# Optimization experiments

Hardware: AMD Instinct MI355X
Metric: run time of the kernel (lower is better)

The kernel has to match this reference:

```python
import jax, jax.numpy as jnp
import numpy as np

B, N, P, D = 16, 1024, 72, 96
ND, H, K = 64, 4, 16
LN_EPS = 1e-5
ROW_EPS = 1e-8


def topk_sparsify(adj, k):
    # adj: (..., N, N); keep top-k per row (scatter-mask), then row-renormalize
    shp = adj.shape
    n = shp[-1]
    flat = adj.reshape(-1, n)
    _, idx = jax.lax.top_k(flat, k)  # (R, k)
    rows = jnp.arange(flat.shape[0])[:, None]
    mask = jnp.zeros_like(flat).at[rows, idx].set(1.0)
    sp = flat * mask
    sp = sp / (sp.sum(-1, keepdims=True) + ROW_EPS)
    return sp.reshape(shp)


def setup_inputs() -> dict:
    key = jax.random.key(0)
    ks = jax.random.split(key, 12)
    xav1 = np.sqrt(6.0 / (N + ND))  # xavier_uniform bound for (N, ND)
    inp = {
        "patch_features": jax.random.normal(ks[0], (B, N, P, D), jnp.float32),
        "E1": jax.random.uniform(ks[1], (H, N, ND), jnp.float32, -xav1, xav1),
        "E2": jax.random.uniform(ks[2], (H, ND, N), jnp.float32, -xav1, xav1),
        "temperature": jnp.full((H,), 0.5, jnp.float32),
        "fusion_weight": jnp.float32(0.5),
        "dW1": jax.random.normal(ks[3], (D, ND), jnp.float32) / np.sqrt(D),
        "db1": jnp.zeros((ND,), jnp.float32),
        "ln_g": jnp.ones((ND,), jnp.float32),
        "ln_b": jnp.zeros((ND,), jnp.float32),
        "dW2": jax.random.normal(ks[4], (ND, ND), jnp.float32) / np.sqrt(ND),
        "db2": jnp.zeros((ND,), jnp.float32),
        "eW1": jax.random.normal(ks[5], (H, 2 * H), jnp.float32) / np.sqrt(H),
        "eb1": jnp.zeros((2 * H,), jnp.float32),
        "eW2": jax.random.normal(ks[6], (2 * H, 1), jnp.float32) / np.sqrt(2 * H),
        "eb2": jnp.zeros((1,), jnp.float32),
    }
    return inp


def reference(patch_features, E1, E2, temperature, fusion_weight,
              dW1, db1, ln_g, ln_b, dW2, db2, eW1, eb1, eW2, eb2):
    # ---- static multi-head graphs: softmax(relu(E1 @ E2) / T, axis=-1) ----
    s = jax.nn.relu(jnp.einsum('hnd,hdm->hnm', E1, E2))
    static_adjs = jax.nn.softmax(s / temperature[:, None, None], axis=-1)

    # ---- dynamic graphs from mean-pooled patch features ----
    node_repr = patch_features.mean(axis=2)                 # (B, N, D)
    h1 = node_repr @ dW1 + db1                              # (B, N, ND)
    mu = h1.mean(-1, keepdims=True)
    var = ((h1 - mu) ** 2).mean(-1, keepdims=True)
    h1 = (h1 - mu) / jnp.sqrt(var + LN_EPS) * ln_g + ln_b   # LayerNorm
    h1 = jax.nn.relu(h1)                                    # (dropout = identity, eval)
    dyn_emb = h1 @ dW2 + db2                                # (B, N, ND)
    d = jax.nn.relu(jnp.einsum('bnd,hdm->bhnm', dyn_emb, E2))
    dynamic_adjs = jax.nn.softmax(d / temperature[None, :, None, None], axis=-1)

    # ---- top-k sparsify + row renormalize ----
    static_adjs = topk_sparsify(static_adjs, K)             # (H, N, N)
    dynamic_adjs = topk_sparsify(dynamic_adjs, K)           # (B, H, N, N)

    # ---- fuse static + dynamic ----
    fused = (1.0 - fusion_weight) * static_adjs[None] + fusion_weight * dynamic_adjs

    # ---- edge MLP over head dim: (B, N, N, H) -> (B, N, N) ----
    x = jnp.transpose(fused, (0, 2, 3, 1))                  # (B, N, N, H)
    ew = jax.nn.relu(x @ eW1 + eb1) @ eW2 + eb2             # (B, N, N, 1)
    final_adjs = jax.nn.sigmoid(ew[..., 0]) * fused.mean(axis=1)
    return final_adjs, static_adjs, dynamic_adjs
```

## Files before the change

kernel.cpp:

```cpp
#include <hip/hip_runtime.h>

typedef unsigned int u32;
typedef unsigned long long u64;

#define Bn 16
#define Nn 1024
#define Pp 72
#define MARG 3e-4f

#define NEGINF __int_as_float(0xff800000)
#define POSINF __int_as_float(0x7f800000)

#define DPP_STEP(OP, CTRL, RM)                                                 \
  y = __builtin_amdgcn_update_dpp(__float_as_int(v), __float_as_int(v),        \
                                  CTRL, RM, 0xf, false);                       \
  v = OP(v, __int_as_float(y));

#define DPP_RED(NAME, OP)                                                      \
  __device__ __forceinline__ float NAME(float v) {                             \
    int y;                                                                     \
    DPP_STEP(OP, 0x111, 0xf)                                                   \
    DPP_STEP(OP, 0x112, 0xf)                                                   \
    DPP_STEP(OP, 0x114, 0xf)                                                   \
    DPP_STEP(OP, 0x118, 0xf)                                                   \
    DPP_STEP(OP, 0x142, 0xa)                                                   \
    DPP_STEP(OP, 0x143, 0xc)                                                   \
    return __int_as_float(__builtin_amdgcn_readlane(__float_as_int(v), 63));   \
  }

#define FADDOP(a, b) ((a) + (b))
DPP_RED(dmaxf, fmaxf)
DPP_RED(dminf, fminf)
DPP_RED(dsumf, FADDOP)

__device__ __forceinline__ u32 wminu(u32 v) {
#pragma unroll
  for (int off = 1; off < 64; off <<= 1) {
    u32 o = (u32)__shfl_xor((int)v, off, 64);
    v = (o < v) ? o : v;
  }
  return v;
}

template <int MODE>
__device__ __forceinline__ void select_row(const float* __restrict__ q,
                                           float* __restrict__ v, int l,
                                           const float* __restrict__ e1row,
                                           const double* __restrict__ edrow,
                                           const float* __restrict__ e2t,
                                           double Td) {
  float lm = q[0];
#pragma unroll
  for (int j = 1; j < 16; ++j) lm = fmaxf(lm, q[j]);
  const float qmax = dmaxf(lm);

  u32 lo = 0u, hi = __float_as_uint(qmax) + 1u;
  u32 kept = 0u;
  bool f16 = false;
  float pvf = 0.0f;
#pragma unroll 1
  while (hi - lo > 1u) {
    u32 mid = (lo + hi) >> 1;
    float pv = __uint_as_float(mid);
    u32 cw = 0;
#pragma unroll
    for (int j = 0; j < 16; ++j)
      cw += (u32)__popcll(__ballot(q[j] >= pv));
    if (cw >= 16u) lo = mid; else hi = mid;
    if (cw == 16u) { f16 = true; pvf = pv; break; }
  }
  float theta, ub;
  if (f16) {
    float vmin = POSINF, umax = -1.0f;
#pragma unroll
    for (int j = 0; j < 16; ++j) {
      if (q[j] >= pvf) { kept |= 1u << j; vmin = fminf(vmin, q[j]); }
      else umax = fmaxf(umax, q[j]);
    }
    theta = dminf(vmin);
    ub = dmaxf(umax);
  } else {
    theta = __uint_as_float(lo);
    u32 cw = 0;
#pragma unroll
    for (int j = 0; j < 16; ++j) {
      cw += (u32)__popcll(__ballot(q[j] > theta));
      if (q[j] > theta) kept |= 1u << j;
    }
    int rr = 16 - (int)cw;
#pragma unroll 1
    for (int it = 0; it < rr; ++it) {
      u32 mc = 0xFFFFFFFFu;
#pragma unroll
      for (int j = 0; j < 16; ++j)
        if (q[j] == theta && !((kept >> j) & 1u)) {
          u32 cc = (u32)((j << 6) | l);
          mc = cc < mc ? cc : mc;
        }
      u32 wm = wminu(mc);
      if ((wm & 63u) == (u32)l) kept |= 1u << (wm >> 6);
    }
    ub = theta;
  }

  if (theta - ub >= MARG) {
    float e[16];
    float es = 0.0f, ek = 0.0f;
#pragma unroll
    for (int j = 0; j < 16; ++j) {
      e[j] = __expf(q[j] - qmax);
      es += e[j];
      if ((kept >> j) & 1u) ek += e[j];
    }
    const float Z = dsumf(es);
    const float EK = dsumf(ek);
    const float inv = 1.0f / (EK + 1e-8f * Z);
#pragma unroll
    for (int j = 0; j < 16; ++j)
      v[j] = ((kept >> j) & 1u) ? (e[j] * inv) : 0.0f;
  } else {
    double qd[16];
    const float thr = ub - MARG;
#pragma unroll 1
    for (int j = 0; j < 16; ++j) {
      if (q[j] >= thr) {
        const int m = l + (j << 6);
        const float* col = e2t + (size_t)m * 64;
        double a = 0.0;
        for (int d = 0; d < 64; ++d) {
          double s = (MODE == 0) ? (double)e1row[d] : edrow[d];
          a = fma(s, (double)col[d], a);
        }
        qd[j] = (a > 0.0 ? a : 0.0) / Td;
      } else {
        qd[j] = (double)q[j];
      }
    }
    double bm = qd[0];
#pragma unroll
    for (int j = 1; j < 16; ++j) bm = qd[j] > bm ? qd[j] : bm;
    float mh = (float)bm;
    float mlo = (float)(bm - (double)mh);
    float whi = dmaxf(mh);
    float wlo = dmaxf(mh == whi ? mlo : NEGINF);
    const double qmaxd = (double)whi + (double)wlo;

    float ev2[16];
    float es2 = 0.0f;
#pragma unroll
    for (int j = 0; j < 16; ++j) { ev2[j] = __expf((float)(qd[j] - qmaxd)); es2 += ev2[j]; }
    const float Z2 = dsumf(es2);

    u32 kept2 = 0;
    float EK2 = 0.0f;
#pragma unroll 1
    for (int it = 0; it < 16; ++it) {
      double bv = -1.0;
      int bjj = -1;
#pragma unroll
      for (int j = 0; j < 16; ++j) {
        bool tk = (((kept2 >> j) & 1u) == 0u) && (qd[j] > bv);
        bv = tk ? qd[j] : bv;
        bjj = tk ? j : bjj;
      }
      float bh = NEGINF, bl = NEGINF;
      if (bjj >= 0) { bh = (float)bv; bl = (float)(bv - (double)bh); }
      float vhi = dmaxf(bh);
      float vlo = dmaxf(bh == vhi ? bl : NEGINF);
      bool elig = (bh == vhi) && (bl == vlo);
      u32 mc = elig ? (u32)((bjj << 6) | l) : 0xFFFFFFFFu;
      u32 mwin = wminu(mc);
      EK2 += __expf((float)(((double)vhi + (double)vlo) - qmaxd));
      if ((mwin & 63u) == (u32)l) kept2 |= 1u << (mwin >> 6);
    }
    const float inv2 = 1.0f / (EK2 + 1e-8f * Z2);
#pragma unroll
    for (int j = 0; j < 16; ++j)
      v[j] = ((kept2 >> j) & 1u) ? (ev2[j] * inv2) : 0.0f;
  }
}

__global__ __launch_bounds__(256) void k_e2t(const float* __restrict__ E2,
                                             float* __restrict__ E2T) {
  __shared__ float tile[32][65];
  const int h = blockIdx.x >> 5;
  const int m0 = (blockIdx.x & 31) << 5;
  const float* src = E2 + (size_t)h * 65536;
  float* dst = E2T + (size_t)h * 65536;
  const int t = threadIdx.x;
#pragma unroll
  for (int k = 0; k < 8; ++k) {
    int idx = k * 256 + t;
    int d = idx >> 5, mm = idx & 31;
    tile[mm][d] = src[d * 1024 + m0 + mm];
  }
  __syncthreads();
#pragma unroll
  for (int k = 0; k < 8; ++k) {
    int idx = k * 256 + t;
    int mm = idx >> 6, d = idx & 63;
    dst[(size_t)(m0 + mm) * 64 + d] = tile[mm][d];
  }
}

__global__ __launch_bounds__(128) void k_meanmlp(const float* __restrict__ pf,
                                                 const float* __restrict__ dW1,
                                                 const float* __restrict__ db1,
                                                 const float* __restrict__ ln_g,
                                                 const float* __restrict__ ln_b,
                                                 const float* __restrict__ dW2,
                                                 const float* __restrict__ db2,
                                                 double* __restrict__ embD,
                                                 float* __restrict__ embF) {
  __shared__ double ndD[96];
  __shared__ double red[64];
  __shared__ double h1r[64];
  const int t = threadIdx.x;
  const int bn = blockIdx.x;

  if (t < 96) {
    const float* src = pf + (size_t)bn * (Pp * 96) + t;
    double s = 0.0;
    for (int p = 0; p < Pp; ++p) s += (double)src[p * 96];
    ndD[t] = s / 72.0;
  }
  __syncthreads();

  double a = 0.0;
  if (t < 64) {
    a = (double)db1[t];
    for (int d = 0; d < 96; ++d) a = fma(ndD[d], (double)dW1[d * 64 + t], a);
    red[t] = a;
  }
  __syncthreads();
  for (int s2 = 32; s2 >= 1; s2 >>= 1) {
    if (t < s2) red[t] += red[t + s2];
    __syncthreads();
  }
  const double mu = red[0] * (1.0 / 64.0);
  __syncthreads();
  const double dv = a - mu;
  if (t < 64) red[t] = dv * dv;
  __syncthreads();
  for (int s2 = 32; s2 >= 1; s2 >>= 1) {
    if (t < s2) red[t] += red[t + s2];
    __syncthreads();
  }
  const double var = red[0] * (1.0 / 64.0);
  if (t < 64) {
    double xn = dv / sqrt(var + 1e-5) * (double)ln_g[t] + (double)ln_b[t];
    h1r[t] = xn > 0.0 ? xn : 0.0;
  }
  __syncthreads();
  if (t < 64) {
    double e = (double)db2[t];
    for (int k = 0; k < 64; ++k) e = fma(h1r[k], (double)dW2[k * 64 + t], e);
    embD[(size_t)bn * 64 + t] = e;
    embF[(size_t)bn * 64 + t] = (float)e;
  }
}

template <int MODE>
__global__ __launch_bounds__(256) void k_dot(const float* __restrict__ e1f,
                                             const float* __restrict__ embF,
                                             const float* __restrict__ E2,
                                             const float* __restrict__ temp,
                                             float* __restrict__ outp) {
  __shared__ float embsh[64][16];
  const int t = threadIdx.x;
  const int r0 = blockIdx.x * 16;
  int h;
  size_t erow;
  if (MODE == 0) {
    h = r0 >> 10;
    erow = (size_t)r0;
  } else {
    int b = r0 >> 12;
    h = (r0 >> 10) & 3;
    int n0 = r0 & 1023;
    erow = (size_t)(b << 10) + n0;
  }
  const float* efa = (MODE == 0) ? (e1f + erow * 64) : (embF + erow * 64);
  const float* e2 = E2 + (size_t)h * 65536;
  const float invT = 1.0f / temp[h];

#pragma unroll
  for (int i = t; i < 1024; i += 256) {
    int g = i & 15, d = i >> 4;
    embsh[d][g] = efa[g * 64 + d];
  }
  __syncthreads();

  const int s = t >> 7;
  const int c1 = (t & 127) * 4;
  const int c2 = c1 + 512;

  float acc[8][8];
#pragma unroll
  for (int g = 0; g < 8; ++g)
#pragma unroll
    for (int x = 0; x < 8; ++x) acc[g][x] = 0.0f;

#pragma unroll 4
  for (int d = 0; d < 64; ++d) {
    float4 va = *(const float4*)(e2 + d * 1024 + c1);
    float4 vb = *(const float4*)(e2 + d * 1024 + c2);
    float4 ea = *(const float4*)&embsh[d][8 * s];
    float4 eb = *(const float4*)&embsh[d][8 * s + 4];
    float sg;
#define ROWFMA(g, SS)                                                          \
    sg = SS;                                                                   \
    acc[g][0] = fmaf(sg, va.x, acc[g][0]);                                     \
    acc[g][1] = fmaf(sg, va.y, acc[g][1]);                                     \
    acc[g][2] = fmaf(sg, va.z, acc[g][2]);                                     \
    acc[g][3] = fmaf(sg, va.w, acc[g][3]);                                     \
    acc[g][4] = fmaf(sg, vb.x, acc[g][4]);                                     \
    acc[g][5] = fmaf(sg, vb.y, acc[g][5]);                                     \
    acc[g][6] = fmaf(sg, vb.z, acc[g][6]);                                     \
    acc[g][7] = fmaf(sg, vb.w, acc[g][7]);
    ROWFMA(0, ea.x) ROWFMA(1, ea.y) ROWFMA(2, ea.z) ROWFMA(3, ea.w)
    ROWFMA(4, eb.x) ROWFMA(5, eb.y) ROWFMA(6, eb.z) ROWFMA(7, eb.w)
#undef ROWFMA
  }

#pragma unroll
  for (int g = 0; g < 8; ++g) {
    float* orow = outp + (size_t)(r0 + 8 * s + g) * 1024;
    float4 o1, o2;
    o1.x = fmaxf(acc[g][0], 0.0f) * invT;
    o1.y = fmaxf(acc[g][1], 0.0f) * invT;
    o1.z = fmaxf(acc[g][2], 0.0f) * invT;
    o1.w = fmaxf(acc[g][3], 0.0f) * invT;
    o2.x = fmaxf(acc[g][4], 0.0f) * invT;
    o2.y = fmaxf(acc[g][5], 0.0f) * invT;
    o2.z = fmaxf(acc[g][6], 0.0f) * invT;
    o2.w = fmaxf(acc[g][7], 0.0f) * invT;
    *(float4*)(orow + c1) = o1;
    *(float4*)(orow + c2) = o2;
  }
}

__global__ __launch_bounds__(256) void k_sel0(const float* __restrict__ E1,
                                              const float* __restrict__ E2T,
                                              const float* __restrict__ temp,
                                              float* __restrict__ outp) {
  const int t = threadIdx.x;
  const int w = t >> 6, l = t & 63;
  const int r = blockIdx.x * 4 + w;
  const int h = r >> 10;
  const float* e2t = E2T + (size_t)h * 65536;
  const double Td = (double)temp[h];
  float* row = outp + (size_t)r * 1024;

  float q[16], v[16];
#pragma unroll
  for (int j = 0; j < 16; ++j) q[j] = row[l + (j << 6)];
  select_row<0>(q, v, l, E1 + (size_t)r * 64, nullptr, e2t, Td);
#pragma unroll
  for (int j = 0; j < 16; ++j) row[l + (j << 6)] = v[j];
}

__global__ __launch_bounds__(256) void k_selfuse(float* __restrict__ dyn,
                                                 const float* __restrict__ stat,
                                                 float* __restrict__ fin,
                                                 const double* __restrict__ embD,
                                                 const float* __restrict__ E2T,
                                                 const float* __restrict__ temp,
                                                 const float* __restrict__ eW1,
                                                 const float* __restrict__ eb1,
                                                 const float* __restrict__ eW2,
                                                 const float* __restrict__ eb2,
                                                 const float* __restrict__ fwp) {
  __shared__ float rowbuf[4][1024];
  const int t = threadIdx.x;
  const int w = t >> 6, l = t & 63;
  const int bn = blockIdx.x;
  const int b = bn >> 10, n = bn & 1023;

  {
    const int h = w;
    float* row = dyn + (((size_t)((b * 4 + h) * 1024 + n)) << 10);
    const float* e2t = E2T + (size_t)h * 65536;
    const double Td = (double)temp[h];
    float q[16], v[16];
#pragma unroll
    for (int j = 0; j < 16; ++j) q[j] = row[l + (j << 6)];
    select_row<1>(q, v, l, nullptr, embD + (((size_t)(b << 10) + n) << 6), e2t, Td);
#pragma unroll
    for (int j = 0; j < 16; ++j) rowbuf[h][l + (j << 6)] = v[j];
  }
  __syncthreads();

#pragma unroll
  for (int k = 0; k < 4; ++k) {
    int idx = t + 256 * k;
    int h2 = idx >> 8, c4 = idx & 255;
    float* drow = dyn + (((size_t)((b * 4 + h2) * 1024 + n)) << 10);
    *(float4*)(drow + c4 * 4) = *(const float4*)&rowbuf[h2][c4 * 4];
  }

  const float fw = fwp[0];
  const float w1 = 1.0f - fw;
  float W1[4][8], B1v[8], W2v[8];
#pragma unroll
  for (int hh = 0; hh < 4; ++hh)
#pragma unroll
    for (int j = 0; j < 8; ++j) W1[hh][j] = eW1[hh * 8 + j];
#pragma unroll
  for (int j = 0; j < 8; ++j) { B1v[j] = eb1[j]; W2v[j] = eW2[j]; }
  const float b2 = eb2[0];

  float fx[4][4];
#pragma unroll
  for (int hh = 0; hh < 4; ++hh) {
    float4 fd = *(const float4*)&rowbuf[hh][t * 4];
    float4 fs = *(const float4*)(stat + (((size_t)(hh * 1024 + n)) << 10) + t * 4);
    fx[hh][0] = w1 * fs.x + fw * fd.x;
    fx[hh][1] = w1 * fs.y + fw * fd.y;
    fx[hh][2] = w1 * fs.z + fw * fd.z;
    fx[hh][3] = w1 * fs.w + fw * fd.w;
  }
  float ov[4];
#pragma unroll
  for (int x = 0; x < 4; ++x) {
    float ew = b2;
#pragma unroll
    for (int j = 0; j < 8; ++j) {
      float hj = B1v[j];
#pragma unroll
      for (int hh = 0; hh < 4; ++hh) hj = fmaf(fx[hh][x], W1[hh][j], hj);
      ew = fmaf(fmaxf(hj, 0.0f), W2v[j], ew);
    }
    float mean = (fx[0][x] + fx[1][x] + fx[2][x] + fx[3][x]) * 0.25f;
    float sg = 1.0f / (1.0f + __expf(-ew));
    ov[x] = sg * mean;
  }
  float4 o;
  o.x = ov[0]; o.y = ov[1]; o.z = ov[2]; o.w = ov[3];
  *(float4*)(fin + (size_t)b * 1048576 + (size_t)n * 1024 + t * 4) = o;
}

extern "C" void kernel_launch(void* const* d_in, const int* in_sizes, int n_in,
                              void* d_out, int out_size, void* d_ws, size_t ws_size,
                              hipStream_t stream) {
  const float* pf   = (const float*)d_in[0];
  const float* E1   = (const float*)d_in[1];
  const float* E2   = (const float*)d_in[2];
  const float* temp = (const float*)d_in[3];
  const float* fw   = (const float*)d_in[4];
  const float* dW1  = (const float*)d_in[5];
  const float* db1  = (const float*)d_in[6];
  const float* ln_g = (const float*)d_in[7];
  const float* ln_b = (const float*)d_in[8];
  const float* dW2  = (const float*)d_in[9];
  const float* db2  = (const float*)d_in[10];
  const float* eW1  = (const float*)d_in[11];
  const float* eb1  = (const float*)d_in[12];
  const float* eW2  = (const float*)d_in[13];
  const float* eb2  = (const float*)d_in[14];

  float* out_final = (float*)d_out;
  float* out_stat  = out_final + (size_t)Bn * Nn * Nn;
  float* out_dyn   = out_stat + (size_t)4 * Nn * Nn;

  double* embD = (double*)d_ws;
  float* embF  = (float*)((char*)d_ws + (8u << 20));
  float* E2T   = (float*)((char*)d_ws + (12u << 20));

  k_e2t<<<128, 256, 0, stream>>>(E2, E2T);
  k_meanmlp<<<Bn * Nn, 128, 0, stream>>>(pf, dW1, db1, ln_g, ln_b, dW2, db2, embD, embF);
  k_dot<0><<<256, 256, 0, stream>>>(E1, nullptr, E2, temp, out_stat);
  k_sel0<<<1024, 256, 0, stream>>>(E1, E2T, temp, out_stat);
  k_dot<1><<<4096, 256, 0, stream>>>(nullptr, embF, E2, temp, out_dyn);
  k_selfuse<<<16384, 256, 0, stream>>>(out_dyn, out_stat, out_final, embD, E2T,
                                       temp, eW1, eb1, eW2, eb2, fw);
}
```

Measured before the change: 542.7 us.

## Fuse logit GEMM with top-k selection and fuse from compact sparse rows

New measurement: 609.0 us. +12.2%, slower.

```diff
diff --git a/kernel.cpp b/kernel.cpp
--- a/kernel.cpp
+++ b/kernel.cpp
@@ -43,12 +43,12 @@
 }
 
 template <int MODE>
-__device__ __forceinline__ void select_row(const float* __restrict__ q,
-                                           float* __restrict__ v, int l,
-                                           const float* __restrict__ e1row,
-                                           const double* __restrict__ edrow,
-                                           const float* __restrict__ e2t,
-                                           double Td) {
+__device__ __forceinline__ u32 select_row(const float* __restrict__ q,
+                                          float* __restrict__ v, int l,
+                                          const float* __restrict__ e1row,
+                                          const double* __restrict__ edrow,
+                                          const float* __restrict__ e2t,
+                                          double Td) {
   float lm = q[0];
 #pragma unroll
   for (int j = 1; j < 16; ++j) lm = fmaxf(lm, q[j]);
@@ -118,6 +118,7 @@
 #pragma unroll
     for (int j = 0; j < 16; ++j)
       v[j] = ((kept >> j) & 1u) ? (e[j] * inv) : 0.0f;
+    return kept;
   } else {
     double qd[16];
     const float thr = ub - MARG;
@@ -177,6 +178,23 @@
 #pragma unroll
     for (int j = 0; j < 16; ++j)
       v[j] = ((kept2 >> j) & 1u) ? (ev2[j] * inv2) : 0.0f;
+    return kept2;
+  }
+}
+
+__device__ __forceinline__ void emit_compact(u32 kept, const float* __restrict__ v,
+                                             int l, float* __restrict__ cbase) {
+  const u64 lt = ((u64)1 << l) - 1;
+  u32 cum = 0;
+#pragma unroll
+  for (int j = 0; j < 16; ++j) {
+    u64 m = __ballot((kept >> j) & 1u);
+    u32 idx = cum + (u32)__popcll(m & lt);
+    if ((kept >> j) & 1u) {
+      cbase[idx] = v[j];
+      cbase[16 + idx] = __uint_as_float((u32)(l + (j << 6)));
+    }
+    cum += (u32)__popcll(m);
   }
 }
 
@@ -261,14 +279,18 @@
 }
 
 template <int MODE>
-__global__ __launch_bounds__(256) void k_dot(const float* __restrict__ e1f,
-                                             const float* __restrict__ embF,
-                                             const float* __restrict__ E2,
-                                             const float* __restrict__ temp,
-                                             float* __restrict__ outp) {
-  __shared__ float embsh[64][16];
+__global__ __launch_bounds__(256) void k_dotsel(const float* __restrict__ e1f,
+                                                const float* __restrict__ embF,
+                                                const double* __restrict__ embD,
+                                                const float* __restrict__ E2,
+                                                const float* __restrict__ E2T,
+                                                const float* __restrict__ temp,
+                                                float* __restrict__ outp,
+                                                float* __restrict__ cmp) {
+  __shared__ float embsh[64][8];
+  __shared__ float lgs[4][1024];
   const int t = threadIdx.x;
-  const int r0 = blockIdx.x * 16;
+  const int r0 = blockIdx.x * 8;
   int h;
   size_t erow;
   if (MODE == 0) {
@@ -282,11 +304,12 @@
   }
   const float* efa = (MODE == 0) ? (e1f + erow * 64) : (embF + erow * 64);
   const float* e2 = E2 + (size_t)h * 65536;
+  const float* e2t = E2T + (size_t)h * 65536;
   const float invT = 1.0f / temp[h];
-
-#pragma unroll
-  for (int i = t; i < 1024; i += 256) {
-    int g = i & 15, d = i >> 4;
+  const double Td = (double)temp[h];
+
+  for (int i = t; i < 512; i += 256) {
+    int g = i & 7, d = i >> 3;
     embsh[d][g] = efa[g * 64 + d];
   }
   __syncthreads();
@@ -295,9 +318,9 @@
   const int c1 = (t & 127) * 4;
   const int c2 = c1 + 512;
 
-  float acc[8][8];
-#pragma unroll
-  for (int g = 0; g < 8; ++g)
+  float acc[4][8];
+#pragma unroll
+  for (int g = 0; g < 4; ++g)
 #pragma unroll
     for (int x = 0; x < 8; ++x) acc[g][x] = 0.0f;
 
@@ -305,8 +328,7 @@
   for (int d = 0; d < 64; ++d) {
     float4 va = *(const float4*)(e2 + d * 1024 + c1);
     float4 vb = *(const float4*)(e2 + d * 1024 + c2);
-    float4 ea = *(const float4*)&embsh[d][8 * s];
-    float4 eb = *(const float4*)&embsh[d][8 * s + 4];
+    float4 ea = *(const float4*)&embsh[d][4 * s];
     float sg;
 #define ROWFMA(g, SS)                                                          \
     sg = SS;                                                                   \
@@ -319,88 +341,84 @@
     acc[g][6] = fmaf(sg, vb.z, acc[g][6]);                                     \
     acc[g][7] = fmaf(sg, vb.w, acc[g][7]);
     ROWFMA(0, ea.x) ROWFMA(1, ea.y) ROWFMA(2, ea.z) ROWFMA(3, ea.w)
-    ROWFMA(4, eb.x) ROWFMA(5, eb.y) ROWFMA(6, eb.z) ROWFMA(7, eb.w)
 #undef ROWFMA
   }
-
-#pragma unroll
-  for (int g = 0; g < 8; ++g) {
-    float* orow = outp + (size_t)(r0 + 8 * s + g) * 1024;
-    float4 o1, o2;
-    o1.x = fmaxf(acc[g][0], 0.0f) * invT;
-    o1.y = fmaxf(acc[g][1], 0.0f) * invT;
-    o1.z = fmaxf(acc[g][2], 0.0f) * invT;
-    o1.w = fmaxf(acc[g][3], 0.0f) * invT;
-    o2.x = fmaxf(acc[g][4], 0.0f) * invT;
-    o2.y = fmaxf(acc[g][5], 0.0f) * invT;
-    o2.z = fmaxf(acc[g][6], 0.0f) * invT;
-    o2.w = fmaxf(acc[g][7], 0.0f) * invT;
-    *(float4*)(orow + c1) = o1;
-    *(float4*)(orow + c2) = o2;
-  }
-}
-
-__global__ __launch_bounds__(256) void k_sel0(const float* __restrict__ E1,
-                                              const float* __restrict__ E2T,
-                                              const float* __restrict__ temp,
-                                              float* __restrict__ outp) {
+#pragma unroll
+  for (int g = 0; g < 4; ++g)
+#pragma unroll
+    for (int x = 0; x < 8; ++x) acc[g][x] = fmaxf(acc[g][x], 0.0f) * invT;
+
+  const int w = t >> 6, l = t & 63;
+
+#pragma unroll
+  for (int gr = 0; gr < 2; ++gr) {
+    if (s == gr) {
+#pragma unroll
+      for (int k = 0; k < 4; ++k) {
+        float4 o1, o2;
+        o1.x = acc[k][0]; o1.y = acc[k][1]; o1.z = acc[k][2]; o1.w = acc[k][3];
+        o2.x = acc[k][4]; o2.y = acc[k][5]; o2.z = acc[k][6]; o2.w = acc[k][7];
+        *(float4*)&lgs[k][c1] = o1;
+        *(float4*)&lgs[k][c2] = o2;
+      }
+    }
+    __syncthreads();
+    {
+      const int rloc = gr * 4 + w;
+      const size_t r = (size_t)r0 + rloc;
+      float q[16], v[16];
+#pragma unroll
+      for (int j = 0; j < 16; ++j) q[j] = lgs[w][l + (j << 6)];
+      u32 kept = select_row<MODE>(
+          q, v, l, (MODE == 0) ? (e1f + r * 64) : nullptr,
+          (MODE == 1) ? (embD + (erow + rloc) * 64) : nullptr, e2t, Td);
+      float* row = outp + r * 1024;
+#pragma unroll
+      for (int j = 0; j < 16; ++j) row[l + (j << 6)] = v[j];
+      emit_compact(kept, v, l, cmp + r * 32);
+    }
+    __syncthreads();
+  }
+}
+
+__global__ __launch_bounds__(256) void k_fusec(const float* __restrict__ cmpd,
+                                               const float* __restrict__ cmp0,
+                                               float* __restrict__ fin,
+                                               const float* __restrict__ eW1,
+                                               const float* __restrict__ eb1,
+                                               const float* __restrict__ eW2,
+                                               const float* __restrict__ eb2,
+                                               const float* __restrict__ fwp) {
+  __shared__ float fused[4][1024];
   const int t = threadIdx.x;
-  const int w = t >> 6, l = t & 63;
-  const int r = blockIdx.x * 4 + w;
-  const int h = r >> 10;
-  const float* e2t = E2T + (size_t)h * 65536;
-  const double Td = (double)temp[h];
-  float* row = outp + (size_t)r * 1024;
-
-  float q[16], v[16];
-#pragma unroll
-  for (int j = 0; j < 16; ++j) q[j] = row[l + (j << 6)];
-  select_row<0>(q, v, l, E1 + (size_t)r * 64, nullptr, e2t, Td);
-#pragma unroll
-  for (int j = 0; j < 16; ++j) row[l + (j << 6)] = v[j];
-}
-
-__global__ __launch_bounds__(256) void k_selfuse(float* __restrict__ dyn,
-                                                 const float* __restrict__ stat,
-                                                 float* __restrict__ fin,
-                                                 const double* __restrict__ embD,
-                                                 const float* __restrict__ E2T,
-                                                 const float* __restrict__ temp,
-                                                 const float* __restrict__ eW1,
-                                                 const float* __restrict__ eb1,
-                                                 const float* __restrict__ eW2,
-                                                 const float* __restrict__ eb2,
-                                                 const float* __restrict__ fwp) {
-  __shared__ float rowbuf[4][1024];
-  const int t = threadIdx.x;
-  const int w = t >> 6, l = t & 63;
   const int bn = blockIdx.x;
   const int b = bn >> 10, n = bn & 1023;
-
-  {
-    const int h = w;
-    float* row = dyn + (((size_t)((b * 4 + h) * 1024 + n)) << 10);
-    const float* e2t = E2T + (size_t)h * 65536;
-    const double Td = (double)temp[h];
-    float q[16], v[16];
-#pragma unroll
-    for (int j = 0; j < 16; ++j) q[j] = row[l + (j << 6)];
-    select_row<1>(q, v, l, nullptr, embD + (((size_t)(b << 10) + n) << 6), e2t, Td);
-#pragma unroll
-    for (int j = 0; j < 16; ++j) rowbuf[h][l + (j << 6)] = v[j];
-  }
-  __syncthreads();
-
-#pragma unroll
-  for (int k = 0; k < 4; ++k) {
-    int idx = t + 256 * k;
-    int h2 = idx >> 8, c4 = idx & 255;
-    float* drow = dyn + (((size_t)((b * 4 + h2) * 1024 + n)) << 10);
-    *(float4*)(drow + c4 * 4) = *(const float4*)&rowbuf[h2][c4 * 4];
-  }
-
   const float fw = fwp[0];
   const float w1 = 1.0f - fw;
+
+  float4* fz = (float4*)&fused[0][0];
+  float4 z; z.x = 0.f; z.y = 0.f; z.z = 0.f; z.w = 0.f;
+#pragma unroll
+  for (int k = 0; k < 4; ++k) fz[t + 256 * k] = z;
+  __syncthreads();
+
+  if (t < 64) {
+    int h = t >> 4, k = t & 15;
+    const float* cb = cmp0 + ((size_t)(h * 1024 + n)) * 32;
+    float val = cb[k];
+    int col = (int)__float_as_uint(cb[16 + k]);
+    fused[h][col] = w1 * val;
+  }
+  __syncthreads();
+  if (t < 64) {
+    int h = t >> 4, k = t & 15;
+    const float* cb = cmpd + ((size_t)((b * 4 + h) * 1024 + n)) * 32;
+    float val = cb[k];
+    int col = (int)__float_as_uint(cb[16 + k]);
+    fused[h][col] += fw * val;
+  }
+  __syncthreads();
+
   float W1[4][8], B1v[8], W2v[8];
 #pragma unroll
   for (int hh = 0; hh < 4; ++hh)
@@ -410,34 +428,28 @@
   for (int j = 0; j < 8; ++j) { B1v[j] = eb1[j]; W2v[j] = eW2[j]; }
   const float b2 = eb2[0];
 
-  float fx[4][4];
-#pragma unroll
-  for (int hh = 0; hh < 4; ++hh) {
-    float4 fd = *(const float4*)&rowbuf[hh][t * 4];
-    float4 fs = *(const float4*)(stat + (((size_t)(hh * 1024 + n)) << 10) + t * 4);
-    fx[hh][0] = w1 * fs.x + fw * fd.x;
-    fx[hh][1] = w1 * fs.y + fw * fd.y;
-    fx[hh][2] = w1 * fs.z + fw * fd.z;
-    fx[hh][3] = w1 * fs.w + fw * fd.w;
-  }
-  float ov[4];
-#pragma unroll
-  for (int x = 0; x < 4; ++x) {
+  float* orow = fin + (size_t)bn * 1024;
+#pragma unroll
+  for (int k = 0; k < 4; ++k) {
+    const int col = t + 256 * k;
+    const float f0 = fused[0][col];
+    const float f1 = fused[1][col];
+    const float f2 = fused[2][col];
+    const float f3 = fused[3][col];
     float ew = b2;
 #pragma unroll
     for (int j = 0; j < 8; ++j) {
       float hj = B1v[j];
-#pragma unroll
-      for (int hh = 0; hh < 4; ++hh) hj = fmaf(fx[hh][x], W1[hh][j], hj);
+      hj = fmaf(f0, W1[0][j], hj);
+      hj = fmaf(f1, W1[1][j], hj);
+      hj = fmaf(f2, W1[2][j], hj);
+      hj = fmaf(f3, W1[3][j], hj);
       ew = fmaf(fmaxf(hj, 0.0f), W2v[j], ew);
     }
-    float mean = (fx[0][x] + fx[1][x] + fx[2][x] + fx[3][x]) * 0.25f;
-    float sg = 1.0f / (1.0f + __expf(-ew));
-    ov[x] = sg * mean;
-  }
-  float4 o;
-  o.x = ov[0]; o.y = ov[1]; o.z = ov[2]; o.w = ov[3];
-  *(float4*)(fin + (size_t)b * 1048576 + (size_t)n * 1024 + t * 4) = o;
+    const float mean = (f0 + f1 + f2 + f3) * 0.25f;
+    const float sg = 1.0f / (1.0f + __expf(-ew));
+    orow[col] = sg * mean;
+  }
 }
 
 extern "C" void kernel_launch(void* const* d_in, const int* in_sizes, int n_in,
@@ -463,15 +475,16 @@
   float* out_stat  = out_final + (size_t)Bn * Nn * Nn;
   float* out_dyn   = out_stat + (size_t)4 * Nn * Nn;
 
-  double* embD = (double*)d_ws;
-  float* embF  = (float*)((char*)d_ws + (8u << 20));
-  float* E2T   = (float*)((char*)d_ws + (12u << 20));
+  char* wsb = (char*)d_ws;
+  double* embD = (double*)wsb;
+  float* embF  = (float*)(wsb + (8u << 20));
+  float* E2T   = (float*)(wsb + (12u << 20));
+  float* cmp0  = (float*)(wsb + (13u << 20));
+  float* cmpd  = (float*)(wsb + (14u << 20));
 
   k_e2t<<<128, 256, 0, stream>>>(E2, E2T);
   k_meanmlp<<<Bn * Nn, 128, 0, stream>>>(pf, dW1, db1, ln_g, ln_b, dW2, db2, embD, embF);
-  k_dot<0><<<256, 256, 0, stream>>>(E1, nullptr, E2, temp, out_stat);
-  k_sel0<<<1024, 256, 0, stream>>>(E1, E2T, temp, out_stat);
-  k_dot<1><<<4096, 256, 0, stream>>>(nullptr, embF, E2, temp, out_dyn);
-  k_selfuse<<<16384, 256, 0, stream>>>(out_dyn, out_stat, out_final, embD, E2T,
-                                       temp, eW1, eb1, eW2, eb2, fw);
-}
+  k_dotsel<0><<<512, 256, 0, stream>>>(E1, nullptr, nullptr, E2, E2T, temp, out_stat, cmp0);
+  k_dotsel<1><<<8192, 256, 0, stream>>>(nullptr, embF, embD, E2, E2T, temp, out_dyn, cmpd);
+  k_fusec<<<16384, 256, 0, stream>>>(cmpd, cmp0, out_final, eW1, eb1, eW2, eb2, fw);
+}
```
